# Optimization experiments

Measured on AMD Instinct MI355X. Metric: run time of the kernel, lower is better.

## Reference

```python
import jax, jax.numpy as jnp
import numpy as np

N_NODES = 50000
N_EDGES = 600000
D_IN = 128
D_OUT = 128


def mean_propagate(x, edge_index, num_nodes):
    # edge_index[0] = source nodes, edge_index[1] = destination nodes
    src, dst = edge_index[0], edge_index[1]
    gathered = x[src]                                   # [E, D]
    summed = jax.ops.segment_sum(gathered, dst, num_segments=num_nodes)  # [N, D]
    deg = jax.ops.segment_sum(jnp.ones((edge_index.shape[1],), dtype=x.dtype), dst,
                              num_segments=num_nodes)   # [N]
    deg = jnp.maximum(deg, 1.0)
    return summed / deg[:, None]


def setup_inputs() -> dict:
    key = jax.random.key(0)
    k1, k2, k3 = jax.random.split(key, 3)
    x = jax.random.normal(k1, (N_NODES, D_IN), dtype=jnp.float32)
    edge_index = jax.random.randint(k2, (2, N_EDGES), 0, N_NODES, dtype=jnp.int64)
    # nn.Linear(in_channels*3, out_channels): weight [out, 3*in], bias [out]
    W = jax.random.normal(k3, (D_OUT, 3 * D_IN), dtype=jnp.float32) / np.sqrt(3 * D_IN)
    b = jnp.zeros((D_OUT,), dtype=jnp.float32)
    return {"x": x, "edge_index": edge_index, "W": W, "b": b}


def reference(x, edge_index, W, b):
    n = x.shape[0]
    hop1 = mean_propagate(x, edge_index, n)
    hop2 = mean_propagate(hop1, edge_index, n)
    feats = jnp.concatenate([x, hop1, hop2], axis=-1)   # [N, 3*D]
    return feats @ W.T + b                              # [N, D_OUT]
```

## Files before the change

kernel.cpp:

```cpp
#include <hip/hip_runtime.h>

#define N_NODES 50000
#define N_EDGES 600000
#define D 128
#define K3 (3 * D)
#define CAP 64
#define NB_G 1563
#define LDSROW 104

typedef __attribute__((ext_vector_type(8))) short short8;
typedef __attribute__((ext_vector_type(4))) float floatx4;
typedef __attribute__((ext_vector_type(8))) unsigned short ushort8;

static __device__ __forceinline__ unsigned short f2bf(float f) {
    unsigned u = __float_as_uint(f);
    u += 0x7fff + ((u >> 16) & 1);
    return (unsigned short)(u >> 16);
}
static __device__ __forceinline__ float bf2f(unsigned short s) {
    return __uint_as_float(((unsigned)s) << 16);
}
static __device__ __forceinline__ unsigned pack2(float a, float b) {
    return (unsigned)f2bf(a) | ((unsigned)f2bf(b) << 16);
}
static __device__ __forceinline__ short8 cvt8(float4 v0, float4 v1) {
    ushort8 o;
    o[0] = f2bf(v0.x); o[1] = f2bf(v0.y); o[2] = f2bf(v0.z); o[3] = f2bf(v0.w);
    o[4] = f2bf(v1.x); o[5] = f2bf(v1.y); o[6] = f2bf(v1.z); o[7] = f2bf(v1.w);
    return *(short8*)&o;
}

__global__ __launch_bounds__(256) void prep_kernel(const float* __restrict__ W,
                                                   unsigned short* __restrict__ Wr,
                                                   int* __restrict__ cnt) {
    const int stride = gridDim.x * 256;
    const int t0 = blockIdx.x * 256 + threadIdx.x;
    for (int i = t0; i < N_NODES + 4; i += stride) cnt[i] = 0;
    for (unsigned id = t0; id < 24u * 4u * 64u; id += stride) {
        unsigned T = id >> 8;
        unsigned ks = (id >> 6) & 3u;
        unsigned lane = id & 63u;
        unsigned c = lane & 15u;
        unsigned q = lane >> 4;
        unsigned row = (T & 7u) * 16u + c;
        unsigned k = (T >> 3) * 128u + ks * 32u + q * 8u;
        const float4 v0 = *(const float4*)(W + (size_t)row * K3 + k);
        const float4 v1 = *(const float4*)(W + (size_t)row * K3 + k + 4);
        short8 o = cvt8(v0, v1);
        *(short8*)(Wr + (size_t)id * 8) = o;
    }
}

__global__ __launch_bounds__(256) void fillb_kernel(const int* __restrict__ src,
                                                    const int* __restrict__ dst,
                                                    int* __restrict__ cnt,
                                                    int* __restrict__ bucket,
                                                    int2* __restrict__ ovf) {
    int* ovfcnt = cnt + N_NODES;
    int e = blockIdx.x * 256 + threadIdx.x;
    if (e < N_EDGES) {
        int d = dst[e];
        int s = src[e];
        int p = atomicAdd(&cnt[d], 1);
        if (p < CAP) bucket[(size_t)d * CAP + p] = s;
        else ovf[atomicAdd(ovfcnt, 1)] = make_int2(d, s);
    }
}

__global__ __launch_bounds__(256) void gemm_kernel(const float* __restrict__ x,
                                                   const unsigned short* __restrict__ Wr,
                                                   const float* __restrict__ bias,
                                                   unsigned short* __restrict__ z) {
    __shared__ unsigned short lds[4 * 32 * LDSROW];
    const int tid = threadIdx.x;
    const int wave = tid >> 6;
    const int lane = tid & 63;
    const int col = lane & 15;
    const int quad = lane >> 4;
    const int mbase = blockIdx.x * 32;
    const int T0 = wave * 6;

    int r0 = mbase + col;
    int r1 = mbase + 16 + col;
    if (r0 >= N_NODES) r0 = N_NODES - 1;
    if (r1 >= N_NODES) r1 = N_NODES - 1;
    const float* ap0 = x + (size_t)r0 * D + quad * 8;
    const float* ap1 = x + (size_t)r1 * D + quad * 8;

    short8 a0r[4], a1r[4];
#pragma unroll
    for (int ks = 0; ks < 4; ++ks) {
        a0r[ks] = cvt8(*(const float4*)(ap0 + ks * 32), *(const float4*)(ap0 + ks * 32 + 4));
        a1r[ks] = cvt8(*(const float4*)(ap1 + ks * 32), *(const float4*)(ap1 + ks * 32 + 4));
    }
    short8 br[24];
#pragma unroll
    for (int t = 0; t < 6; ++t)
#pragma unroll
        for (int ks = 0; ks < 4; ++ks)
            br[t * 4 + ks] = *(const short8*)(Wr + (size_t)(((T0 + t) * 4 + ks) * 64 + lane) * 8);

    floatx4 acc0[6], acc1[6];
#pragma unroll
    for (int t = 0; t < 6; ++t) {
        acc0[t] = (floatx4){0.f, 0.f, 0.f, 0.f};
        acc1[t] = (floatx4){0.f, 0.f, 0.f, 0.f};
    }
#pragma unroll
    for (int ks = 0; ks < 4; ++ks) {
#pragma unroll
        for (int t = 0; t < 6; ++t) {
            acc0[t] = __builtin_amdgcn_mfma_f32_16x16x32_bf16(br[t * 4 + ks], a0r[ks], acc0[t], 0, 0, 0);
            acc1[t] = __builtin_amdgcn_mfma_f32_16x16x32_bf16(br[t * 4 + ks], a1r[ks], acc1[t], 0, 0, 0);
        }
    }

    unsigned short* wlds = lds + wave * 32 * LDSROW;
#pragma unroll
    for (int t = 0; t < 6; ++t) {
        int T = T0 + t;
        float4 bq = (float4){0.f, 0.f, 0.f, 0.f};
        if (T < 8) bq = *(const float4*)(bias + T * 16 + quad * 4);
        uint2 p;
        p.x = pack2(acc0[t][0] + bq.x, acc0[t][1] + bq.y);
        p.y = pack2(acc0[t][2] + bq.z, acc0[t][3] + bq.w);
        *(uint2*)(wlds + col * LDSROW + t * 16 + quad * 4) = p;
        uint2 q2;
        q2.x = pack2(acc1[t][0] + bq.x, acc1[t][1] + bq.y);
        q2.y = pack2(acc1[t][2] + bq.z, acc1[t][3] + bq.w);
        *(uint2*)(wlds + (col + 16) * LDSROW + t * 16 + quad * 4) = q2;
    }
    __syncthreads();
#pragma unroll
    for (int it = 0; it < 6; ++it) {
        int id = it * 256 + tid;
        int row = id / 48;
        int ch = id - row * 48;
        int w = ch / 12;
        int cc = (ch - w * 12) * 8;
        int node = mbase + row;
        ushort8 v = *(const ushort8*)(lds + (size_t)w * 32 * LDSROW + row * LDSROW + cc);
        if (node < N_NODES)
            *(ushort8*)(z + (size_t)node * K3 + ch * 8) = v;
    }
}

__global__ __launch_bounds__(256) void gather1_kernel(const unsigned short* __restrict__ z,
                                                      const int* __restrict__ cnt,
                                                      const int* __restrict__ bucket,
                                                      const int2* __restrict__ ovf,
                                                      unsigned short* __restrict__ tb) {
    unsigned n = (blockIdx.x * 256 + threadIdx.x) >> 6;
    if (n >= N_NODES) return;
    const int lane = threadIdx.x & 63;
    const int s = lane >> 4;
    const unsigned c = (lane & 15u) << 3;
    const unsigned short* fin = z + 256 + c;
    const int deg = cnt[n];
    const int dcap = min(deg, CAP);
    const int* bp = bucket + (size_t)n * CAP;
    float acc[8] = {0.f, 0.f, 0.f, 0.f, 0.f, 0.f, 0.f, 0.f};
    for (int base = s * 4; base < dcap; base += 16) {
        int4 idx = *(const int4*)(bp + base);
        float m0 = 1.f;
        float m1 = (base + 1 < dcap) ? 1.f : 0.f;
        float m2 = (base + 2 < dcap) ? 1.f : 0.f;
        float m3 = (base + 3 < dcap) ? 1.f : 0.f;
        int s0 = min(max(idx.x, 0), N_NODES - 1);
        int s1 = min(max(idx.y, 0), N_NODES - 1);
        int s2 = min(max(idx.z, 0), N_NODES - 1);
        int s3 = min(max(idx.w, 0), N_NODES - 1);
        ushort8 v0 = *(const ushort8*)(fin + (size_t)s0 * K3);
        ushort8 v1 = *(const ushort8*)(fin + (size_t)s1 * K3);
        ushort8 v2 = *(const ushort8*)(fin + (size_t)s2 * K3);
        ushort8 v3 = *(const ushort8*)(fin + (size_t)s3 * K3);
#pragma unroll
        for (int j = 0; j < 8; ++j)
            acc[j] += (m0 * bf2f(v0[j]) + m1 * bf2f(v1[j])) +
                      (m2 * bf2f(v2[j]) + m3 * bf2f(v3[j]));
    }
    if (deg > CAP) {
        int oc = cnt[N_NODES];
        if (s == 0)
            for (int i = 0; i < oc; ++i) {
                int2 p = ovf[i];
                if (p.x == (int)n) {
                    ushort8 v = *(const ushort8*)(fin + (size_t)p.y * K3);
#pragma unroll
                    for (int j = 0; j < 8; ++j) acc[j] += bf2f(v[j]);
                }
            }
    }
#pragma unroll
    for (int j = 0; j < 8; ++j) {
        acc[j] += __shfl_xor(acc[j], 16);
        acc[j] += __shfl_xor(acc[j], 32);
    }
    if (s == 0) {
        float inv = 1.0f / fmaxf((float)deg, 1.0f);
        ushort8 za = *(const ushort8*)(z + (size_t)n * K3 + 128 + c);
        ushort8 o;
#pragma unroll
        for (int j = 0; j < 8; ++j) o[j] = f2bf(bf2f(za[j]) + acc[j] * inv);
        *(ushort8*)(tb + (size_t)n * D + c) = o;
    }
}

__global__ __launch_bounds__(256) void gather2_kernel(const unsigned short* __restrict__ z,
                                                      const unsigned short* __restrict__ tb,
                                                      const int* __restrict__ cnt,
                                                      const int* __restrict__ bucket,
                                                      const int2* __restrict__ ovf,
                                                      float* __restrict__ out) {
    unsigned n = (blockIdx.x * 256 + threadIdx.x) >> 6;
    if (n >= N_NODES) return;
    const int lane = threadIdx.x & 63;
    const int s = lane >> 4;
    const unsigned c = (lane & 15u) << 3;
    const unsigned short* fin = tb + c;
    const int deg = cnt[n];
    const int dcap = min(deg, CAP);
    const int* bp = bucket + (size_t)n * CAP;
    float acc[8] = {0.f, 0.f, 0.f, 0.f, 0.f, 0.f, 0.f, 0.f};
    for (int base = s * 4; base < dcap; base += 16) {
        int4 idx = *(const int4*)(bp + base);
        float m0 = 1.f;
        float m1 = (base + 1 < dcap) ? 1.f : 0.f;
        float m2 = (base + 2 < dcap) ? 1.f : 0.f;
        float m3 = (base + 3 < dcap) ? 1.f : 0.f;
        int s0 = min(max(idx.x, 0), N_NODES - 1);
        int s1 = min(max(idx.y, 0), N_NODES - 1);
        int s2 = min(max(idx.z, 0), N_NODES - 1);
        int s3 = min(max(idx.w, 0), N_NODES - 1);
        ushort8 v0 = *(const ushort8*)(fin + (size_t)s0 * D);
        ushort8 v1 = *(const ushort8*)(fin + (size_t)s1 * D);
        ushort8 v2 = *(const ushort8*)(fin + (size_t)s2 * D);
        ushort8 v3 = *(const ushort8*)(fin + (size_t)s3 * D);
#pragma unroll
        for (int j = 0; j < 8; ++j)
            acc[j] += (m0 * bf2f(v0[j]) + m1 * bf2f(v1[j])) +
                      (m2 * bf2f(v2[j]) + m3 * bf2f(v3[j]));
    }
    if (deg > CAP) {
        int oc = cnt[N_NODES];
        if (s == 0)
            for (int i = 0; i < oc; ++i) {
                int2 p = ovf[i];
                if (p.x == (int)n) {
                    ushort8 v = *(const ushort8*)(fin + (size_t)p.y * D);
#pragma unroll
                    for (int j = 0; j < 8; ++j) acc[j] += bf2f(v[j]);
                }
            }
    }
#pragma unroll
    for (int j = 0; j < 8; ++j) {
        acc[j] += __shfl_xor(acc[j], 16);
        acc[j] += __shfl_xor(acc[j], 32);
    }
    if (s == 0) {
        float inv = 1.0f / fmaxf((float)deg, 1.0f);
        ushort8 za = *(const ushort8*)(z + (size_t)n * K3 + c);
        float4 q0, q1;
        q0.x = bf2f(za[0]) + acc[0] * inv;
        q0.y = bf2f(za[1]) + acc[1] * inv;
        q0.z = bf2f(za[2]) + acc[2] * inv;
        q0.w = bf2f(za[3]) + acc[3] * inv;
        q1.x = bf2f(za[4]) + acc[4] * inv;
        q1.y = bf2f(za[5]) + acc[5] * inv;
        q1.z = bf2f(za[6]) + acc[6] * inv;
        q1.w = bf2f(za[7]) + acc[7] * inv;
        *(float4*)(out + (size_t)n * D + c) = q0;
        *(float4*)(out + (size_t)n * D + c + 4) = q1;
    }
}

extern "C" void kernel_launch(void* const* d_in, const int* in_sizes, int n_in,
                              void* d_out, int out_size, void* d_ws, size_t ws_size,
                              hipStream_t stream) {
    const float* x = (const float*)d_in[0];
    const int* ei = (const int*)d_in[1];
    const float* W = (const float*)d_in[2];
    const float* b = (const float*)d_in[3];
    float* out = (float*)d_out;
    const int* src = ei;
    const int* dst = ei + N_EDGES;

    unsigned short* z = (unsigned short*)d_ws;
    unsigned short* tb = z + (size_t)N_NODES * K3;
    unsigned short* Wr = tb + (size_t)N_NODES * D;
    int* cnt = (int*)(Wr + 6144 * 8);
    int* bucket = cnt + N_NODES + 4;
    int2* ovf = (int2*)(bucket + (size_t)N_NODES * CAP);

    prep_kernel<<<200, 256, 0, stream>>>(W, Wr, cnt);
    fillb_kernel<<<(N_EDGES + 255) / 256, 256, 0, stream>>>(src, dst, cnt, bucket, ovf);
    gemm_kernel<<<NB_G, 256, 0, stream>>>(x, Wr, b, z);

    const int ggrid = (N_NODES * 64 + 255) / 256;
    gather1_kernel<<<ggrid, 256, 0, stream>>>(z, cnt, bucket, ovf, tb);
    gather2_kernel<<<ggrid, 256, 0, stream>>>(z, tb, cnt, bucket, ovf, out);
}
```

Baseline: 190.4 us.

## Fuse edge bucketing into the GEMM kernel to drop a launch

Moves the per-edge atomic bucketing work from its own kernel into the GEMM kernel. Each of the 1563 GEMM blocks also handles 384 edges, placed after the operand loads so the atomics can overlap with MFMA work. This removes one kernel launch and lets the scatter latency hide behind compute, at the cost of extra register pressure and memory traffic inside the GEMM kernel.

```diff
diff --git a/kernel.cpp b/kernel.cpp
--- a/kernel.cpp
+++ b/kernel.cpp
@@ -6,6 +6,7 @@
 #define K3 (3 * D)
 #define CAP 64
 #define NB_G 1563
+#define EPB 384
 #define LDSROW 104
 
 typedef __attribute__((ext_vector_type(8))) short short8;
@@ -51,26 +52,15 @@
     }
 }
 
-__global__ __launch_bounds__(256) void fillb_kernel(const int* __restrict__ src,
-                                                    const int* __restrict__ dst,
-                                                    int* __restrict__ cnt,
-                                                    int* __restrict__ bucket,
-                                                    int2* __restrict__ ovf) {
-    int* ovfcnt = cnt + N_NODES;
-    int e = blockIdx.x * 256 + threadIdx.x;
-    if (e < N_EDGES) {
-        int d = dst[e];
-        int s = src[e];
-        int p = atomicAdd(&cnt[d], 1);
-        if (p < CAP) bucket[(size_t)d * CAP + p] = s;
-        else ovf[atomicAdd(ovfcnt, 1)] = make_int2(d, s);
-    }
-}
-
-__global__ __launch_bounds__(256) void gemm_kernel(const float* __restrict__ x,
-                                                   const unsigned short* __restrict__ Wr,
-                                                   const float* __restrict__ bias,
-                                                   unsigned short* __restrict__ z) {
+__global__ __launch_bounds__(256) void gemmfill_kernel(const float* __restrict__ x,
+                                                       const unsigned short* __restrict__ Wr,
+                                                       const float* __restrict__ bias,
+                                                       const int* __restrict__ src,
+                                                       const int* __restrict__ dst,
+                                                       int* __restrict__ cnt,
+                                                       int* __restrict__ bucket,
+                                                       int2* __restrict__ ovf,
+                                                       unsigned short* __restrict__ z) {
     __shared__ unsigned short lds[4 * 32 * LDSROW];
     const int tid = threadIdx.x;
     const int wave = tid >> 6;
@@ -99,6 +89,29 @@
 #pragma unroll
         for (int ks = 0; ks < 4; ++ks)
             br[t * 4 + ks] = *(const short8*)(Wr + (size_t)(((T0 + t) * 4 + ks) * 64 + lane) * 8);
+
+    {
+        int* ovfcnt = cnt + N_NODES;
+        const int ebase = blockIdx.x * EPB;
+        int e0 = ebase + tid;
+        if (e0 < N_EDGES) {
+            int d = dst[e0];
+            int s = src[e0];
+            int p = atomicAdd(&cnt[d], 1);
+            if (p < CAP) bucket[(size_t)d * CAP + p] = s;
+            else ovf[atomicAdd(ovfcnt, 1)] = make_int2(d, s);
+        }
+        if (tid < EPB - 256) {
+            int e1 = ebase + 256 + tid;
+            if (e1 < N_EDGES) {
+                int d = dst[e1];
+                int s = src[e1];
+                int p = atomicAdd(&cnt[d], 1);
+                if (p < CAP) bucket[(size_t)d * CAP + p] = s;
+                else ovf[atomicAdd(ovfcnt, 1)] = make_int2(d, s);
+            }
+        }
+    }
 
     floatx4 acc0[6], acc1[6];
 #pragma unroll
@@ -294,8 +307,7 @@
     int2* ovf = (int2*)(bucket + (size_t)N_NODES * CAP);
 
     prep_kernel<<<200, 256, 0, stream>>>(W, Wr, cnt);
-    fillb_kernel<<<(N_EDGES + 255) / 256, 256, 0, stream>>>(src, dst, cnt, bucket, ovf);
-    gemm_kernel<<<NB_G, 256, 0, stream>>>(x, Wr, b, z);
+    gemmfill_kernel<<<NB_G, 256, 0, stream>>>(x, Wr, b, src, dst, cnt, bucket, ovf, z);
 
     const int ggrid = (N_NODES * 64 + 255) / 256;
     gather1_kernel<<<ggrid, 256, 0, stream>>>(z, cnt, bucket, ovf, tb);
```

Result: faster. 175.0 us (-8.1%).
